# Kernel optimization log

Hardware: AMD Instinct MI355X
Metric: run time of the kernel (lower is better)

The kernel has to match this reference:

```python
import math
import jax, jax.numpy as jnp
import numpy as np

B, S, D, H = 4, 1024, 768, 12  # batch, seq, hidden, heads (ViT-Base)
HD = D // H                     # head size = 64
EPS = 1e-12                     # F.normalize eps


def setup_inputs() -> dict:
    key = jax.random.key(0)
    ks = jax.random.split(key, 7)
    s = 0.02
    return {
        "hidden_states": jax.random.normal(ks[0], (B, S, D), dtype=jnp.float32),
        "Wq": jax.random.normal(ks[1], (D, D), dtype=jnp.float32) * s,
        "bq": jax.random.normal(ks[2], (D,), dtype=jnp.float32) * s,
        "Wv": jax.random.normal(ks[3], (D, D), dtype=jnp.float32) * s,
        "bv": jax.random.normal(ks[4], (D,), dtype=jnp.float32) * s,
        "Wo": jax.random.normal(ks[5], (D, D), dtype=jnp.float32) * s,
        "bo": jax.random.normal(ks[6], (D,), dtype=jnp.float32) * s,
    }


def _split_heads(x):
    # [B,S,D] -> [B,H,S,hd]
    b, s, _ = x.shape
    return x.reshape(b, s, H, HD).transpose(0, 2, 1, 3)


def reference(hidden_states, Wq, bq, Wv, bv, Wo, bo):
    b, s, d_model = hidden_states.shape
    # Linear layers (torch Linear: x @ W^T + b; here W stored already transposed)
    mixed_q = hidden_states @ Wq + bq          # key == query in this module
    mixed_v = hidden_states @ Wv + bv
    q = _split_heads(mixed_q)                  # [B,H,S,hd]
    v = _split_heads(mixed_v)                  # [B,H,S,hd]

    # symmetric self-attention (Q @ Q^T)
    scores = jnp.einsum("bhsd,bhtd->bhst", q, q) / math.sqrt(HD)
    probs1 = jax.nn.softmax(scores, axis=-1)                 # [B,H,S,S]
    probs = 0.5 * (probs1 + probs1.transpose(0, 1, 3, 2))    # symmetrize

    # F.normalize(value_layer, dim=2): L2-normalize along the SEQUENCE axis
    vnorm = jnp.maximum(jnp.sqrt(jnp.sum(v * v, axis=2, keepdims=True)), EPS)
    V = v / vnorm                                            # [B,H,S,hd]

    # random-walk Laplacian: D^{-1}(D - P) = I - P / rowsum  (diag structure exploited,
    # same math as diag_embed + matmul in the original)
    dvec = probs.sum(axis=3)                                 # [B,H,S]
    Pn = probs / dvec[..., :, None]                          # D^{-1} P
    LrwV = V - jnp.einsum("bhst,bhtd->bhsd", Pn, V)          # L_rw @ V

    # trace( sum_{b,h} V^T L_rw V ) = sum over all (b,h,s,d) of V * (L_rw V)
    denom = jnp.float32(HD * H * b)
    tr = jnp.abs(jnp.sum(V * LrwV)) / denom

    # orthogonality regularizer: sum (V^T V - I)^2
    VtV = jnp.einsum("bhsd,bhse->bhde", V, V)                # [B,H,hd,hd]
    regular_term = jnp.sum((VtV - jnp.eye(HD, dtype=V.dtype)) ** 2) / denom

    # context = P @ V  (is_last=False)
    ctx = jnp.einsum("bhst,bhtd->bhsd", probs, v)
    ctx = ctx.transpose(0, 2, 1, 3).reshape(b, s, d_model)
    attention_output = ctx @ Wo + bo                         # dropout = identity (p=0)
    return (attention_output, tr, regular_term, mixed_q, mixed_q)
```

## Files before the change

kernel.cpp:

```cpp
#include <hip/hip_runtime.h>
#include <math.h>

constexpr float SCALE = 0.125f;

typedef __attribute__((ext_vector_type(8))) short bf8;
typedef __attribute__((ext_vector_type(8))) unsigned short u16x8;
typedef __attribute__((ext_vector_type(4))) float f32x4;

static __device__ __forceinline__ unsigned short f2bf(float f) {
    unsigned int u = __float_as_uint(f);
    u += 0x7fffu + ((u >> 16) & 1u);
    return (unsigned short)(u >> 16);
}
static __device__ __forceinline__ float bf2f(unsigned short h) {
    return __uint_as_float(((unsigned int)h) << 16);
}
static __device__ __forceinline__ bf8 ld8(const unsigned short* p) {
    return *reinterpret_cast<const bf8*>(p);
}
static __device__ __forceinline__ unsigned int cvtpk(float lo, float hi) {
    unsigned int r;
    asm("v_cvt_pk_bf16_f32 %0, %1, %2" : "=v"(r) : "v"(lo), "v"(hi));
    return r;
}

__global__ __launch_bounds__(256)
void k_prep(const float* __restrict__ Wq, const float* __restrict__ Wv,
            unsigned short* __restrict__ WTq, unsigned short* __restrict__ WTv)
{
    __shared__ unsigned short T[64 * 72];
    const int bid = blockIdx.x;
    const bool isQ = (bid < 144);
    const int lb = isQ ? bid : bid - 144;
    const float* __restrict__ W = isQ ? Wq : Wv;
    unsigned short* __restrict__ WT = isQ ? WTq : WTv;
    const int n0 = (lb % 12) * 64;
    const int k0 = (lb / 12) * 64;
    const int tid = threadIdx.x;
    const int r  = tid >> 2;
    const int c0 = (tid & 3) * 16;
    const float* src = &W[(size_t)(k0 + r) * 768 + n0 + c0];
    #pragma unroll
    for (int q = 0; q < 4; ++q) {
        const float4 v = *reinterpret_cast<const float4*>(src + q * 4);
        uint2 pk;
        pk.x = cvtpk(v.x, v.y);
        pk.y = cvtpk(v.z, v.w);
        *reinterpret_cast<uint2*>(&T[r * 72 + c0 + q * 4]) = pk;
    }
    __syncthreads();
    const int n  = tid >> 2;
    const int kc = (tid & 3) * 16;
    u16x8 o0, o1;
    #pragma unroll
    for (int i = 0; i < 8; ++i) o0[i] = T[(kc + i) * 72 + n];
    #pragma unroll
    for (int i = 0; i < 8; ++i) o1[i] = T[(kc + 8 + i) * 72 + n];
    unsigned short* dst = WT + (size_t)(n0 + n) * 768 + k0 + kc;
    *reinterpret_cast<u16x8*>(dst)     = o0;
    *reinterpret_cast<u16x8*>(dst + 8) = o1;
}

__global__ __launch_bounds__(256)
void k_gemm_qv(const float* __restrict__ X,
               const unsigned short* __restrict__ WTq,
               const unsigned short* __restrict__ WTv,
               const float* __restrict__ bq, const float* __restrict__ bv,
               float* __restrict__ mq1, float* __restrict__ mq2,
               unsigned short* __restrict__ qb, unsigned short* __restrict__ mvb)
{
    __shared__ unsigned short As[64 * 72];
    __shared__ unsigned short Bs[128 * 72];
    const int m0 = blockIdx.x * 64;
    const bool isQ = (blockIdx.y < 6);
    const int n0 = (isQ ? blockIdx.y : blockIdx.y - 6) * 128;
    const unsigned short* __restrict__ WT = isQ ? WTq : WTv;
    const float* __restrict__ bias = isQ ? bq : bv;
    const int tid = threadIdx.x;
    const int wave = tid >> 6, lane = tid & 63, lm = lane & 15, lg = lane >> 4;
    const int wn = wave;

    f32x4 acc[4][2];
    #pragma unroll
    for (int mi = 0; mi < 4; ++mi)
        #pragma unroll
        for (int ni = 0; ni < 2; ++ni) acc[mi][ni] = (f32x4){0.f, 0.f, 0.f, 0.f};

    for (int k0 = 0; k0 < 768; k0 += 64) {
        #pragma unroll
        for (int it = 0; it < 4; ++it) {
            const int idx = tid + it * 256;
            const int arow = idx >> 4;
            const int ac4  = (idx & 15) * 4;
            const float4 v = *reinterpret_cast<const float4*>(
                &X[(size_t)(m0 + arow) * 768 + k0 + ac4]);
            uint2 pk;
            pk.x = cvtpk(v.x, v.y);
            pk.y = cvtpk(v.z, v.w);
            *reinterpret_cast<uint2*>(&As[arow * 72 + ac4]) = pk;
            const int brow = idx >> 3;
            const int bc8  = (idx & 7) * 8;
            *reinterpret_cast<u16x8*>(&Bs[brow * 72 + bc8]) =
                *reinterpret_cast<const u16x8*>(&WT[(size_t)(n0 + brow) * 768 + k0 + bc8]);
        }
        __syncthreads();
        #pragma unroll
        for (int ks = 0; ks < 2; ++ks) {
            bf8 af[4], bfr[2];
            #pragma unroll
            for (int mi = 0; mi < 4; ++mi)
                af[mi] = *reinterpret_cast<const bf8*>(
                    &As[(mi * 16 + lm) * 72 + ks * 32 + lg * 8]);
            #pragma unroll
            for (int ni = 0; ni < 2; ++ni)
                bfr[ni] = *reinterpret_cast<const bf8*>(
                    &Bs[(wn * 32 + ni * 16 + lm) * 72 + ks * 32 + lg * 8]);
            #pragma unroll
            for (int mi = 0; mi < 4; ++mi)
                #pragma unroll
                for (int ni = 0; ni < 2; ++ni)
                    acc[mi][ni] = __builtin_amdgcn_mfma_f32_16x16x32_bf16(
                        af[mi], bfr[ni], acc[mi][ni], 0, 0, 0);
        }
        __syncthreads();
    }
    #pragma unroll
    for (int ni = 0; ni < 2; ++ni) {
        const int c = n0 + wn * 32 + ni * 16 + lm;
        const float bcol = bias[c];
        #pragma unroll
        for (int mi = 0; mi < 4; ++mi)
            #pragma unroll
            for (int j = 0; j < 4; ++j) {
                const int r = m0 + mi * 16 + lg * 4 + j;
                const float v = acc[mi][ni][j] + bcol;
                const size_t off = (size_t)r * 768 + c;
                if (isQ) {
                    mq1[off] = v;
                    mq2[off] = v;
                    qb[off]  = f2bf(v);
                } else {
                    mvb[off] = f2bf(v);
                }
            }
    }
}

__global__ __launch_bounds__(256)
void k_gemm_one(const unsigned short* __restrict__ Xb,
                const unsigned short* __restrict__ WT,
                const float* __restrict__ bias, float* __restrict__ out,
                const float* __restrict__ t1p, const float* __restrict__ t2p,
                const float* __restrict__ regp, float* __restrict__ out_tr,
                float* __restrict__ out_reg)
{
    __shared__ unsigned short As[64 * 72];
    __shared__ unsigned short Bs[64 * 72];
    __shared__ float R1[256];
    __shared__ float R2[256];
    __shared__ float R3[256];
    const int tid = threadIdx.x;

    if (blockIdx.x == 768) {
        float s1 = 0.f, s2 = 0.f, s3 = 0.f;
        for (int i = tid; i < 768; i += 256) s2 += t2p[i];
        if (tid < 48) { s1 = t1p[tid]; s3 = regp[tid]; }
        R1[tid] = s1; R2[tid] = s2; R3[tid] = s3;
        __syncthreads();
        for (int w = 128; w >= 1; w >>= 1) {
            if (tid < w) { R1[tid] += R1[tid + w]; R2[tid] += R2[tid + w]; R3[tid] += R3[tid + w]; }
            __syncthreads();
        }
        if (tid == 0) {
            *out_tr  = fabsf(R1[0] - R2[0]) / 3072.f;
            *out_reg = R3[0] / 3072.f;
        }
        return;
    }

    const int m0 = (blockIdx.x & 63) * 64;
    const int n0 = (blockIdx.x >> 6) * 64;
    const int w = tid >> 6, lane = tid & 63, lm = lane & 15, lg = lane >> 4;

    f32x4 acc[4];
    #pragma unroll
    for (int ni = 0; ni < 4; ++ni) acc[ni] = (f32x4){0.f, 0.f, 0.f, 0.f};

    for (int k0 = 0; k0 < 768; k0 += 64) {
        #pragma unroll
        for (int it = 0; it < 2; ++it) {
            const int idx = tid + it * 256;
            const int row = idx >> 3;
            const int c8  = (idx & 7) * 8;
            *reinterpret_cast<u16x8*>(&As[row * 72 + c8]) =
                *reinterpret_cast<const u16x8*>(&Xb[(size_t)(m0 + row) * 768 + k0 + c8]);
            *reinterpret_cast<u16x8*>(&Bs[row * 72 + c8]) =
                *reinterpret_cast<const u16x8*>(&WT[(size_t)(n0 + row) * 768 + k0 + c8]);
        }
        __syncthreads();
        #pragma unroll
        for (int ks = 0; ks < 2; ++ks) {
            const bf8 af = *reinterpret_cast<const bf8*>(
                &As[(w * 16 + lm) * 72 + ks * 32 + lg * 8]);
            #pragma unroll
            for (int ni = 0; ni < 4; ++ni) {
                const bf8 bfr = *reinterpret_cast<const bf8*>(
                    &Bs[(ni * 16 + lm) * 72 + ks * 32 + lg * 8]);
                acc[ni] = __builtin_amdgcn_mfma_f32_16x16x32_bf16(af, bfr, acc[ni], 0, 0, 0);
            }
        }
        __syncthreads();
    }
    #pragma unroll
    for (int ni = 0; ni < 4; ++ni) {
        const int c = n0 + ni * 16 + lm;
        const float bcol = bias[c];
        #pragma unroll
        for (int j = 0; j < 4; ++j) {
            const int r = m0 + w * 16 + lg * 4 + j;
            out[(size_t)r * 768 + c] = acc[ni][j] + bcol;
        }
    }
}

__global__ __launch_bounds__(256)
void k_pass1T(const unsigned short* __restrict__ qb,
              const unsigned short* __restrict__ mvb,
              unsigned short* __restrict__ vT,
              float* __restrict__ a, float* __restrict__ nrmp)
{
    __shared__ __align__(16) unsigned short Kb[2][128 * 72];
    const int bid = blockIdx.x;
    const int st = (bid >> 3) & 15;
    const int bh = (bid & 7) + 8 * (bid >> 7);
    const int b = bh / 12, h = bh % 12;
    const int s0 = st * 64;
    const int tid = threadIdx.x;
    const int w = tid >> 6, lane = tid & 63, lm = lane & 15, lg = lane >> 4;
    const size_t qoff = (size_t)(b * 1024) * 768 + h * 64;

    {
        const int r  = tid >> 2;
        const int c0 = (tid & 3) * 16;
        const unsigned short* src = mvb + (size_t)(b * 1024 + s0 + r) * 768 + h * 64 + c0;
        const u16x8 x0 = *reinterpret_cast<const u16x8*>(src);
        const u16x8 x1 = *reinterpret_cast<const u16x8*>(src + 8);
        *reinterpret_cast<u16x8*>(&Kb[0][r * 72 + c0])     = x0;
        *reinterpret_cast<u16x8*>(&Kb[0][r * 72 + c0 + 8]) = x1;
        __syncthreads();
        const int dd  = tid >> 2;
        const int sc0 = (tid & 3) * 16;
        u16x8 o0, o1;
        float ps = 0.f;
        #pragma unroll
        for (int k = 0; k < 8; ++k) {
            o0[k] = Kb[0][(sc0 + k) * 72 + dd];
            const float v = bf2f(o0[k]);
            ps = fmaf(v, v, ps);
        }
        #pragma unroll
        for (int k = 0; k < 8; ++k) {
            o1[k] = Kb[0][(sc0 + 8 + k) * 72 + dd];
            const float v = bf2f(o1[k]);
            ps = fmaf(v, v, ps);
        }
        ps += __shfl_xor(ps, 1);
        ps += __shfl_xor(ps, 2);
        if ((tid & 3) == 0) nrmp[(size_t)(bh * 16 + st) * 64 + dd] = ps;
        unsigned short* dst = vT + (size_t)bh * 65536 + (size_t)dd * 1024 + s0 + sc0;
        *reinterpret_cast<u16x8*>(dst)     = o0;
        *reinterpret_cast<u16x8*>(dst + 8) = o1;
        __syncthreads();
    }

    const unsigned short* srow_p = qb + qoff + (size_t)(s0 + 16 * w + lm) * 768;
    const bf8 qs0 = ld8(srow_p + 8 * lg);
    const bf8 qs1 = ld8(srow_p + 32 + 8 * lg);
    const f32x4 z = {0.f, 0.f, 0.f, 0.f};
    float r = 0.f;

    u16x8 kr[4];
    #pragma unroll
    for (int it = 0; it < 4; ++it) {
        const int idx = tid + it * 256;
        kr[it] = *reinterpret_cast<const u16x8*>(
            qb + qoff + (size_t)(idx >> 3) * 768 + (idx & 7) * 8);
    }
    #pragma unroll
    for (int it = 0; it < 4; ++it) {
        const int idx = tid + it * 256;
        *reinterpret_cast<u16x8*>(&Kb[0][(idx >> 3) * 72 + (idx & 7) * 8]) = kr[it];
    }
    __syncthreads();
    int cur = 0;

    for (int tt = 0; tt < 8; ++tt) {
        const bool pf = (tt < 7);
        if (pf) {
            #pragma unroll
            for (int it = 0; it < 4; ++it) {
                const int idx = tid + it * 256;
                kr[it] = *reinterpret_cast<const u16x8*>(
                    qb + qoff + (size_t)((tt + 1) * 128 + (idx >> 3)) * 768 + (idx & 7) * 8);
            }
        }
        #pragma unroll
        for (int nf = 0; nf < 8; ++nf) {
            const bf8 ka0 = *reinterpret_cast<const bf8*>(
                &Kb[cur][(16 * nf + lm) * 72 + 8 * lg]);
            const bf8 ka1 = *reinterpret_cast<const bf8*>(
                &Kb[cur][(16 * nf + lm) * 72 + 32 + 8 * lg]);
            f32x4 ef = __builtin_amdgcn_mfma_f32_16x16x32_bf16(ka0, qs0, z, 0, 0, 0);
            ef = __builtin_amdgcn_mfma_f32_16x16x32_bf16(ka1, qs1, ef, 0, 0, 0);
            r += __expf(ef[0] * SCALE) + __expf(ef[1] * SCALE)
               + __expf(ef[2] * SCALE) + __expf(ef[3] * SCALE);
        }
        if (pf) {
            #pragma unroll
            for (int it = 0; it < 4; ++it) {
                const int idx = tid + it * 256;
                *reinterpret_cast<u16x8*>(
                    &Kb[cur ^ 1][(idx >> 3) * 72 + (idx & 7) * 8]) = kr[it];
            }
        }
        __syncthreads();
        cur ^= 1;
    }
    r += __shfl_xor(r, 16);
    r += __shfl_xor(r, 32);
    if (lg == 0) a[(size_t)bh * 1024 + s0 + 16 * w + lm] = 1.f / r;
}

__global__ __launch_bounds__(256)
void k_pass2(const unsigned short* __restrict__ qb,
             const unsigned short* __restrict__ vT,
             const unsigned short* __restrict__ mvb,
             const float* __restrict__ a,
             const float* __restrict__ nrmp,
             float* __restrict__ invn_out,
             unsigned short* __restrict__ ctxb,
             float* __restrict__ t2p)
{
    __shared__ __align__(16) unsigned short Kb[2][64 * 72];
    __shared__ __align__(16) unsigned short Vb[2][64 * 72];
    __shared__ __align__(16) unsigned short F_lds[4 * 16 * 72];
    __shared__ float red[256];
    __shared__ float inv_sh[64];
    const int bid = blockIdx.x;
    const int st = (bid >> 3) & 15;
    const int bh = (bid & 7) + 8 * (bid >> 7);
    const int b = bh / 12, h = bh % 12;
    const int s0 = st * 64;
    const int tid = threadIdx.x;
    const int w = tid >> 6, lane = tid & 63, lm = lane & 15, lg = lane >> 4;
    const size_t qoff = (size_t)(b * 1024) * 768 + h * 64;
    const unsigned short* srow_p = qb + qoff + (size_t)(s0 + 16 * w + lm) * 768;
    const bf8 qs0 = ld8(srow_p + 8 * lg);
    const bf8 qs1 = ld8(srow_p + 32 + 8 * lg);
    const unsigned short* vbase = vT + (size_t)bh * 65536;
    const float* abase = a + (size_t)bh * 1024;
    const float a_s = abase[s0 + 16 * w + lm];
    unsigned short* Frow = &F_lds[w * 1152 + lm * 72];
    const f32x4 z = {0.f, 0.f, 0.f, 0.f};
    f32x4 acc[4];
    #pragma unroll
    for (int nf = 0; nf < 4; ++nf) acc[nf] = z;
    float sF = 0.f;
    const int sr = tid >> 2;
    const int sc = (tid & 3) << 4;

    if (tid < 64) {
        float s = 0.f;
        #pragma unroll
        for (int t = 0; t < 16; ++t) s += nrmp[(size_t)(bh * 16 + t) * 64 + tid];
        const float iv = 1.f / fmaxf(sqrtf(s), 1e-12f);
        inv_sh[tid] = iv;
        if (st == 0) invn_out[bh * 64 + tid] = iv;
    }

    u16x8 kr0 = *reinterpret_cast<const u16x8*>(qb + qoff + (size_t)sr * 768 + sc);
    u16x8 kr1 = *reinterpret_cast<const u16x8*>(qb + qoff + (size_t)sr * 768 + sc + 8);
    u16x8 vr0 = *reinterpret_cast<const u16x8*>(vbase + (size_t)sr * 1024 + sc);
    u16x8 vr1 = *reinterpret_cast<const u16x8*>(vbase + (size_t)sr * 1024 + sc + 8);
    *reinterpret_cast<u16x8*>(&Kb[0][sr * 72 + sc])     = kr0;
    *reinterpret_cast<u16x8*>(&Kb[0][sr * 72 + sc + 8]) = kr1;
    *reinterpret_cast<u16x8*>(&Vb[0][sr * 72 + sc])     = vr0;
    *reinterpret_cast<u16x8*>(&Vb[0][sr * 72 + sc + 8]) = vr1;
    __syncthreads();
    int cur = 0;

    for (int tt = 0; tt < 16; ++tt) {
        const int t0 = tt * 64;
        if (tt < 15) {
            const size_t kg = qoff + (size_t)(t0 + 64 + sr) * 768 + sc;
            kr0 = *reinterpret_cast<const u16x8*>(qb + kg);
            kr1 = *reinterpret_cast<const u16x8*>(qb + kg + 8);
            const size_t vg = (size_t)sr * 1024 + t0 + 64 + sc;
            vr0 = *reinterpret_cast<const u16x8*>(vbase + vg);
            vr1 = *reinterpret_cast<const u16x8*>(vbase + vg + 8);
        }
        f32x4 ef[4];
        #pragma unroll
        for (int nf = 0; nf < 4; ++nf) {
            const bf8 ka0 = *reinterpret_cast<const bf8*>(
                &Kb[cur][(16 * nf + lm) * 72 + 8 * lg]);
            const bf8 ka1 = *reinterpret_cast<const bf8*>(
                &Kb[cur][(16 * nf + lm) * 72 + 32 + 8 * lg]);
            ef[nf] = __builtin_amdgcn_mfma_f32_16x16x32_bf16(ka0, qs0, z, 0, 0, 0);
            ef[nf] = __builtin_amdgcn_mfma_f32_16x16x32_bf16(ka1, qs1, ef[nf], 0, 0, 0);
        }
        #pragma unroll
        for (int nf = 0; nf < 4; ++nf) {
            const float4 af = *reinterpret_cast<const float4*>(
                abase + t0 + 16 * nf + 4 * lg);
            const float f0 = __expf(ef[nf][0] * SCALE) * (a_s + af.x);
            const float f1 = __expf(ef[nf][1] * SCALE) * (a_s + af.y);
            const float f2 = __expf(ef[nf][2] * SCALE) * (a_s + af.z);
            const float f3 = __expf(ef[nf][3] * SCALE) * (a_s + af.w);
            sF += (f0 + f1) + (f2 + f3);
            uint2 pk;
            pk.x = cvtpk(f0, f1);
            pk.y = cvtpk(f2, f3);
            *reinterpret_cast<uint2*>(&Frow[16 * nf + 4 * lg]) = pk;
        }
        #pragma unroll
        for (int ks = 0; ks < 2; ++ks) {
            const bf8 fa = *reinterpret_cast<const bf8*>(&Frow[32 * ks + 8 * lg]);
            #pragma unroll
            for (int nf = 0; nf < 4; ++nf) {
                const bf8 vfr = *reinterpret_cast<const bf8*>(
                    &Vb[cur][(16 * nf + lm) * 72 + 32 * ks + 8 * lg]);
                acc[nf] = __builtin_amdgcn_mfma_f32_16x16x32_bf16(fa, vfr, acc[nf], 0, 0, 0);
            }
        }
        if (tt < 15) {
            *reinterpret_cast<u16x8*>(&Kb[cur ^ 1][sr * 72 + sc])     = kr0;
            *reinterpret_cast<u16x8*>(&Kb[cur ^ 1][sr * 72 + sc + 8]) = kr1;
            *reinterpret_cast<u16x8*>(&Vb[cur ^ 1][sr * 72 + sc])     = vr0;
            *reinterpret_cast<u16x8*>(&Vb[cur ^ 1][sr * 72 + sc + 8]) = vr1;
        }
        __syncthreads();
        cur ^= 1;
    }
    sF += __shfl_xor(sF, 16);
    sF += __shfl_xor(sF, 32);

    float t2 = 0.f;
    #pragma unroll
    for (int j = 0; j < 4; ++j) {
        const int srow = s0 + 16 * w + 4 * lg + j;
        const float sFj = __shfl(sF, 4 * lg + j);
        const float rdv = 2.f / sFj;
        const size_t rowoff = (size_t)(b * 1024 + srow) * 768 + h * 64;
        #pragma unroll
        for (int nf = 0; nf < 4; ++nf) {
            const int d = lm + 16 * nf;
            const float iv = inv_sh[d];
            const float cf = 0.5f * acc[nf][j];
            ctxb[rowoff + d] = f2bf(cf);
            const float vv = bf2f(mvb[rowoff + d]);
            t2 = fmaf(vv * cf, iv * iv * rdv, t2);
        }
    }
    red[tid] = t2;
    __syncthreads();
    for (int k = 128; k >= 1; k >>= 1) {
        if (tid < k) red[tid] += red[tid + k];
        __syncthreads();
    }
    if (tid == 0) t2p[bh * 16 + st] = red[0];
}

__global__ __launch_bounds__(256)
void k_regwt(const unsigned short* __restrict__ vT, float* __restrict__ Gpart,
             const float* __restrict__ Wo, unsigned short* __restrict__ WTo)
{
    __shared__ unsigned short T[64 * 72];
    const int bid = blockIdx.x;
    const int tid = threadIdx.x;
    if (bid < 384) {
        const int bh = bid >> 3;
        const int q  = bid & 7;
        const int w = tid >> 6, lane = tid & 63, lm = lane & 15, lg = lane >> 4;
        const unsigned short* base = vT + (size_t)bh * 65536;
        const unsigned short* arowp = base + (size_t)(16 * w + lm) * 1024;
        const f32x4 z = {0.f, 0.f, 0.f, 0.f};
        f32x4 acc[4];
        #pragma unroll
        for (int nf = 0; nf < 4; ++nf) acc[nf] = z;
        #pragma unroll
        for (int kk = 0; kk < 4; ++kk) {
            const int t0 = (q * 4 + kk) * 32 + 8 * lg;
            const bf8 av = ld8(arowp + t0);
            #pragma unroll
            for (int nf = 0; nf < 4; ++nf) {
                const bf8 bv = ld8(base + (size_t)(lm + 16 * nf) * 1024 + t0);
                acc[nf] = __builtin_amdgcn_mfma_f32_16x16x32_bf16(av, bv, acc[nf], 0, 0, 0);
            }
        }
        float* gdst = Gpart + (size_t)(bh * 8 + q) * 4096;
        #pragma unroll
        for (int nf = 0; nf < 4; ++nf) {
            const int d2 = lm + 16 * nf;
            #pragma unroll
            for (int j = 0; j < 4; ++j) {
                const int d1 = 16 * w + 4 * lg + j;
                gdst[d1 * 64 + d2] = acc[nf][j];
            }
        }
    } else {
        const int lb = bid - 384;
        const int n0 = (lb % 12) * 64;
        const int k0 = (lb / 12) * 64;
        const int r  = tid >> 2;
        const int c0 = (tid & 3) * 16;
        const float* src = &Wo[(size_t)(k0 + r) * 768 + n0 + c0];
        #pragma unroll
        for (int q = 0; q < 4; ++q) {
            const float4 v = *reinterpret_cast<const float4*>(src + q * 4);
            uint2 pk;
            pk.x = cvtpk(v.x, v.y);
            pk.y = cvtpk(v.z, v.w);
            *reinterpret_cast<uint2*>(&T[r * 72 + c0 + q * 4]) = pk;
        }
        __syncthreads();
        const int n  = tid >> 2;
        const int kc = (tid & 3) * 16;
        u16x8 o0, o1;
        #pragma unroll
        for (int i = 0; i < 8; ++i) o0[i] = T[(kc + i) * 72 + n];
        #pragma unroll
        for (int i = 0; i < 8; ++i) o1[i] = T[(kc + 8 + i) * 72 + n];
        unsigned short* dst = WTo + (size_t)(n0 + n) * 768 + k0 + kc;
        *reinterpret_cast<u16x8*>(dst)     = o0;
        *reinterpret_cast<u16x8*>(dst + 8) = o1;
    }
}

__global__ __launch_bounds__(256)
void k_regfin(const float* __restrict__ Gpart, const float* __restrict__ invn,
              const float* __restrict__ nrmp,
              float* __restrict__ regp, float* __restrict__ t1p)
{
    const int bh = blockIdx.x;
    const int tid = threadIdx.x;
    float part = 0.f;
    for (int c = tid; c < 4096; c += 256) {
        const int d1 = c >> 6, d2 = c & 63;
        float g = 0.f;
        #pragma unroll
        for (int q = 0; q < 8; ++q)
            g += Gpart[(size_t)(bh * 8 + q) * 4096 + c];
        g *= invn[bh * 64 + d1] * invn[bh * 64 + d2];
        const float diff = g - ((d1 == d2) ? 1.f : 0.f);
        part = fmaf(diff, diff, part);
    }
    float t1l = 0.f;
    if (tid < 64) {
        float s = 0.f;
        #pragma unroll
        for (int t = 0; t < 16; ++t) s += nrmp[(size_t)(bh * 16 + t) * 64 + tid];
        const float iv = invn[bh * 64 + tid];
        t1l = s * iv * iv;
    }
    __shared__ float red[256];
    __shared__ float redT[256];
    red[tid] = part;
    redT[tid] = t1l;
    __syncthreads();
    for (int k = 128; k >= 1; k >>= 1) {
        if (tid < k) { red[tid] += red[tid + k]; redT[tid] += redT[tid + k]; }
        __syncthreads();
    }
    if (tid == 0) { regp[bh] = red[0]; t1p[bh] = redT[0]; }
}

extern "C" void kernel_launch(void* const* d_in, const int* in_sizes, int n_in,
                              void* d_out, int out_size, void* d_ws, size_t ws_size,
                              hipStream_t stream)
{
    const float* X  = (const float*)d_in[0];
    const float* Wq = (const float*)d_in[1];
    const float* bq = (const float*)d_in[2];
    const float* Wv = (const float*)d_in[3];
    const float* bv = (const float*)d_in[4];
    const float* Wo = (const float*)d_in[5];
    const float* bo = (const float*)d_in[6];

    float* out = (float*)d_out;
    float* att = out;
    float* tr  = out + 3145728;
    float* rg  = out + 3145729;
    float* mq1 = out + 3145730;
    float* mq2 = out + 6291458;

    float* ws = (float*)d_ws;
    unsigned short* mvb  = (unsigned short*)(ws);
    unsigned short* WTo  = (unsigned short*)(ws);
    unsigned short* qb   = (unsigned short*)(ws + 1572864);
    float*          Gpart = ws + 1572864;
    unsigned short* vTslot = (unsigned short*)(ws + 3145728);
    unsigned short* WTq  = vTslot;
    unsigned short* WTv  = vTslot + 589824;
    unsigned short* vT   = vTslot;
    unsigned short* ctxb = (unsigned short*)(ws + 4718592);
    float* nrmp = ws + 6291456;
    float* aarr = ws + 6389760;
    float* invn = ws + 6438960;
    float* t1p  = ws + 6442032;
    float* t2p  = ws + 6442080;
    float* regp = ws + 6442848;

    if (ws_size < (size_t)6442896 * sizeof(float)) return;

    k_prep     <<<288,          256, 0, stream>>>(Wq, Wv, WTq, WTv);
    k_gemm_qv  <<<dim3(64, 12), 256, 0, stream>>>(X, WTq, WTv, bq, bv, mq1, mq2, qb, mvb);
    k_pass1T   <<<768,          256, 0, stream>>>(qb, mvb, vT, aarr, nrmp);
    k_pass2    <<<768,          256, 0, stream>>>(qb, vT, mvb, aarr, nrmp, invn, ctxb, t2p);
    k_regwt    <<<528,          256, 0, stream>>>(vT, Gpart, Wo, WTo);
    k_regfin   <<<48,           256, 0, stream>>>(Gpart, invn, nrmp, regp, t1p);
    k_gemm_one <<<769,          256, 0, stream>>>(ctxb, WTo, bo, att,
                                                  t1p, t2p, regp, tr, rg);
}
```

Measured before the change: 118.4 us.

## Register-prefetch next K tile and double K-step size in QV and output GEMMs

Both projection GEMMs now use a K step of 128 instead of 64, halving the number of barrier-separated iterations. Global loads for the next tile are issued into registers before the MFMA work on the current tile, then written to shared memory after a barrier. The goal is to overlap global-memory latency with compute and cut synchronisation count. The cost is more registers for the staging buffers and roughly double the shared memory per block, which may lower occupancy.

```diff
diff --git a/kernel.cpp b/kernel.cpp
--- a/kernel.cpp
+++ b/kernel.cpp
@@ -69,8 +69,8 @@
                float* __restrict__ mq1, float* __restrict__ mq2,
                unsigned short* __restrict__ qb, unsigned short* __restrict__ mvb)
 {
-    __shared__ unsigned short As[64 * 72];
-    __shared__ unsigned short Bs[128 * 72];
+    __shared__ unsigned short As[64 * 136];
+    __shared__ unsigned short Bs[128 * 136];
     const int m0 = blockIdx.x * 64;
     const bool isQ = (blockIdx.y < 6);
     const int n0 = (isQ ? blockIdx.y : blockIdx.y - 6) * 128;
@@ -86,41 +86,70 @@
         #pragma unroll
         for (int ni = 0; ni < 2; ++ni) acc[mi][ni] = (f32x4){0.f, 0.f, 0.f, 0.f};
 
-    for (int k0 = 0; k0 < 768; k0 += 64) {
-        #pragma unroll
-        for (int it = 0; it < 4; ++it) {
-            const int idx = tid + it * 256;
-            const int arow = idx >> 4;
-            const int ac4  = (idx & 15) * 4;
-            const float4 v = *reinterpret_cast<const float4*>(
-                &X[(size_t)(m0 + arow) * 768 + k0 + ac4]);
-            uint2 pk;
-            pk.x = cvtpk(v.x, v.y);
-            pk.y = cvtpk(v.z, v.w);
-            *reinterpret_cast<uint2*>(&As[arow * 72 + ac4]) = pk;
-            const int brow = idx >> 3;
-            const int bc8  = (idx & 7) * 8;
-            *reinterpret_cast<u16x8*>(&Bs[brow * 72 + bc8]) =
-                *reinterpret_cast<const u16x8*>(&WT[(size_t)(n0 + brow) * 768 + k0 + bc8]);
-        }
-        __syncthreads();
-        #pragma unroll
-        for (int ks = 0; ks < 2; ++ks) {
+    float4 ar[8];
+    u16x8  br[8];
+
+    #pragma unroll
+    for (int it = 0; it < 8; ++it) {
+        const int idx = tid + it * 256;
+        ar[it] = *reinterpret_cast<const float4*>(
+            &X[(size_t)(m0 + (idx >> 5)) * 768 + (idx & 31) * 4]);
+        br[it] = *reinterpret_cast<const u16x8*>(
+            &WT[(size_t)(n0 + (idx >> 4)) * 768 + (idx & 15) * 8]);
+    }
+    #pragma unroll
+    for (int it = 0; it < 8; ++it) {
+        const int idx = tid + it * 256;
+        uint2 pk;
+        pk.x = cvtpk(ar[it].x, ar[it].y);
+        pk.y = cvtpk(ar[it].z, ar[it].w);
+        *reinterpret_cast<uint2*>(&As[(idx >> 5) * 136 + (idx & 31) * 4]) = pk;
+        *reinterpret_cast<u16x8*>(&Bs[(idx >> 4) * 136 + (idx & 15) * 8]) = br[it];
+    }
+    __syncthreads();
+
+    for (int step = 0; step < 6; ++step) {
+        const bool pf = (step < 5);
+        if (pf) {
+            const int k0 = (step + 1) * 128;
+            #pragma unroll
+            for (int it = 0; it < 8; ++it) {
+                const int idx = tid + it * 256;
+                ar[it] = *reinterpret_cast<const float4*>(
+                    &X[(size_t)(m0 + (idx >> 5)) * 768 + k0 + (idx & 31) * 4]);
+                br[it] = *reinterpret_cast<const u16x8*>(
+                    &WT[(size_t)(n0 + (idx >> 4)) * 768 + k0 + (idx & 15) * 8]);
+            }
+        }
+        #pragma unroll
+        for (int ks = 0; ks < 4; ++ks) {
             bf8 af[4], bfr[2];
             #pragma unroll
             for (int mi = 0; mi < 4; ++mi)
                 af[mi] = *reinterpret_cast<const bf8*>(
-                    &As[(mi * 16 + lm) * 72 + ks * 32 + lg * 8]);
+                    &As[(mi * 16 + lm) * 136 + ks * 32 + lg * 8]);
             #pragma unroll
             for (int ni = 0; ni < 2; ++ni)
                 bfr[ni] = *reinterpret_cast<const bf8*>(
-                    &Bs[(wn * 32 + ni * 16 + lm) * 72 + ks * 32 + lg * 8]);
+                    &Bs[(wn * 32 + ni * 16 + lm) * 136 + ks * 32 + lg * 8]);
             #pragma unroll
             for (int mi = 0; mi < 4; ++mi)
                 #pragma unroll
                 for (int ni = 0; ni < 2; ++ni)
                     acc[mi][ni] = __builtin_amdgcn_mfma_f32_16x16x32_bf16(
                         af[mi], bfr[ni], acc[mi][ni], 0, 0, 0);
+        }
+        __syncthreads();
+        if (pf) {
+            #pragma unroll
+            for (int it = 0; it < 8; ++it) {
+                const int idx = tid + it * 256;
+                uint2 pk;
+                pk.x = cvtpk(ar[it].x, ar[it].y);
+                pk.y = cvtpk(ar[it].z, ar[it].w);
+                *reinterpret_cast<uint2*>(&As[(idx >> 5) * 136 + (idx & 31) * 4]) = pk;
+                *reinterpret_cast<u16x8*>(&Bs[(idx >> 4) * 136 + (idx & 15) * 8]) = br[it];
+            }
         }
         __syncthreads();
     }
@@ -154,8 +183,8 @@
                 const float* __restrict__ regp, float* __restrict__ out_tr,
                 float* __restrict__ out_reg)
 {
-    __shared__ unsigned short As[64 * 72];
-    __shared__ unsigned short Bs[64 * 72];
+    __shared__ unsigned short As[64 * 136];
+    __shared__ unsigned short Bs[64 * 136];
     __shared__ float R1[256];
     __shared__ float R2[256];
     __shared__ float R3[256];
@@ -186,27 +215,54 @@
     #pragma unroll
     for (int ni = 0; ni < 4; ++ni) acc[ni] = (f32x4){0.f, 0.f, 0.f, 0.f};
 
-    for (int k0 = 0; k0 < 768; k0 += 64) {
-        #pragma unroll
-        for (int it = 0; it < 2; ++it) {
-            const int idx = tid + it * 256;
-            const int row = idx >> 3;
-            const int c8  = (idx & 7) * 8;
-            *reinterpret_cast<u16x8*>(&As[row * 72 + c8]) =
-                *reinterpret_cast<const u16x8*>(&Xb[(size_t)(m0 + row) * 768 + k0 + c8]);
-            *reinterpret_cast<u16x8*>(&Bs[row * 72 + c8]) =
-                *reinterpret_cast<const u16x8*>(&WT[(size_t)(n0 + row) * 768 + k0 + c8]);
-        }
-        __syncthreads();
-        #pragma unroll
-        for (int ks = 0; ks < 2; ++ks) {
+    u16x8 ara[4], arb[4];
+    #pragma unroll
+    for (int it = 0; it < 4; ++it) {
+        const int idx = tid + it * 256;
+        ara[it] = *reinterpret_cast<const u16x8*>(
+            &Xb[(size_t)(m0 + (idx >> 4)) * 768 + (idx & 15) * 8]);
+        arb[it] = *reinterpret_cast<const u16x8*>(
+            &WT[(size_t)(n0 + (idx >> 4)) * 768 + (idx & 15) * 8]);
+    }
+    #pragma unroll
+    for (int it = 0; it < 4; ++it) {
+        const int idx = tid + it * 256;
+        *reinterpret_cast<u16x8*>(&As[(idx >> 4) * 136 + (idx & 15) * 8]) = ara[it];
+        *reinterpret_cast<u16x8*>(&Bs[(idx >> 4) * 136 + (idx & 15) * 8]) = arb[it];
+    }
+    __syncthreads();
+
+    for (int step = 0; step < 6; ++step) {
+        const bool pf = (step < 5);
+        if (pf) {
+            const int k0 = (step + 1) * 128;
+            #pragma unroll
+            for (int it = 0; it < 4; ++it) {
+                const int idx = tid + it * 256;
+                ara[it] = *reinterpret_cast<const u16x8*>(
+                    &Xb[(size_t)(m0 + (idx >> 4)) * 768 + k0 + (idx & 15) * 8]);
+                arb[it] = *reinterpret_cast<const u16x8*>(
+                    &WT[(size_t)(n0 + (idx >> 4)) * 768 + k0 + (idx & 15) * 8]);
+            }
+        }
+        #pragma unroll
+        for (int ks = 0; ks < 4; ++ks) {
             const bf8 af = *reinterpret_cast<const bf8*>(
-                &As[(w * 16 + lm) * 72 + ks * 32 + lg * 8]);
+                &As[(w * 16 + lm) * 136 + ks * 32 + lg * 8]);
             #pragma unroll
             for (int ni = 0; ni < 4; ++ni) {
                 const bf8 bfr = *reinterpret_cast<const bf8*>(
-                    &Bs[(ni * 16 + lm) * 72 + ks * 32 + lg * 8]);
+                    &Bs[(ni * 16 + lm) * 136 + ks * 32 + lg * 8]);
                 acc[ni] = __builtin_amdgcn_mfma_f32_16x16x32_bf16(af, bfr, acc[ni], 0, 0, 0);
+            }
+        }
+        __syncthreads();
+        if (pf) {
+            #pragma unroll
+            for (int it = 0; it < 4; ++it) {
+                const int idx = tid + it * 256;
+                *reinterpret_cast<u16x8*>(&As[(idx >> 4) * 136 + (idx & 15) * 8]) = ara[it];
+                *reinterpret_cast<u16x8*>(&Bs[(idx >> 4) * 136 + (idx & 15) * 8]) = arb[it];
             }
         }
         __syncthreads();
```

Result: slower. 123.0 us (+3.9%).
